# Kernel optimization log

Hardware: AMD Instinct MI355X
Metric: run time of the kernel (lower is better)

Reference implementation:

```python
import jax, jax.numpy as jnp
import numpy as np

K = 2           # top-k experts
TEMP = 1.0      # router temperature


def setup_inputs() -> dict:
    key = jax.random.key(0)
    k0, k1, k2, k3 = jax.random.split(key, 4)
    B, T, C, E = 4, 8192, 1024, 64
    x = jax.random.normal(k0, (B, T, C), dtype=jnp.float32)
    cond = jax.random.normal(k1, (B, C), dtype=jnp.float32)
    # nn.Linear weights: gate (E, C), cond_proj (C, 2C)
    Wg = jax.random.normal(k2, (E, C), dtype=jnp.float32) * 0.02
    Wc = jax.random.normal(k3, (C, 2 * C), dtype=jnp.float32) * 0.02
    return {"x": x, "cond": cond, "Wg": Wg, "Wc": Wc}


def reference(x, cond, Wg, Wc):
    B, T, C = x.shape
    E = Wg.shape[0]
    # conditioning path: broadcast cond over tokens, concat, project
    c_exp = jnp.broadcast_to(cond[:, None, :], (B, T, C))
    hc = jnp.concatenate([x, c_exp], axis=-1)          # (B,T,2C)
    h = jnp.einsum('btd,cd->btc', hc, Wc)              # (B,T,C)
    logits = jnp.einsum('btc,ec->bte', h, Wg) * (1.0 / TEMP)  # (B,T,E)
    probs = jax.nn.softmax(logits, axis=-1)
    topk_vals, idx = jax.lax.top_k(logits, K)          # (B,T,K), sorted desc
    scores = jax.nn.softmax(topk_vals, axis=-1)
    # aux stats (no_grad in torch)
    importance = jax.lax.stop_gradient(jnp.mean(probs, axis=(0, 1)))  # (E,)
    counts = jnp.zeros((E,), probs.dtype).at[idx.reshape(-1)].add(1.0)
    load = counts / jnp.clip(jnp.sum(counts), 1.0)
    load = jax.lax.stop_gradient(load)
    return (idx, scores, probs, importance, load)
```

## Files before the change

### kernel.cpp

```cpp
#include <hip/hip_runtime.h>
#include <math.h>

#define B_    4
#define T_    8192
#define C_    1024
#define E_    64
#define NTOK  (B_*T_)
#define KSEL  2

#define OFF_IDX    0
#define OFF_SCORES (NTOK*KSEL)
#define OFF_PROBS  (2*NTOK*KSEL)
#define OFF_IMP    (OFF_PROBS + NTOK*E_)
#define OFF_LOAD   (OFF_IMP + E_)

#define WS_WCOMB64 0
#define WS_HCOND64 524288
#define WS_LBIAS64 557056
#define WS_WCOMB32 559104
#define WS_LBIAS32 821248
#define WS_CNT     822272
#define WS_LIST    822784

#define REFINE_CAP 4096
#define REFINE_EPS 3e-4f

__global__ __launch_bounds__(256) void k_wcomb(const float* __restrict__ Wg,
                                               const float* __restrict__ Wc,
                                               double* __restrict__ wcomb64,
                                               float* __restrict__ wcomb32) {
    __shared__ float wg_s[64 * 65];
    __shared__ float wc_s[64 * 4];
    const int tid = threadIdx.x;
    const int e  = tid & 63;
    const int dl = tid >> 6;
    const int d  = blockIdx.x * 4 + dl;

    double acc = 0.0;
    for (int c0 = 0; c0 < C_; c0 += 64) {
        __syncthreads();
#pragma unroll
        for (int k = 0; k < 16; ++k) {
            int li = tid + k * 256;
            int el = li >> 6, cc = li & 63;
            wg_s[el * 65 + cc] = Wg[el * 1024 + c0 + cc];
        }
        {
            int cc = tid >> 2, dd = tid & 3;
            wc_s[cc * 4 + dd] = Wc[(size_t)(c0 + cc) * 2048 + blockIdx.x * 4 + dd];
        }
        __syncthreads();
#pragma unroll 4
        for (int cc = 0; cc < 64; ++cc) {
            acc += (double)wc_s[cc * 4 + dl] * (double)wg_s[e * 65 + cc];
        }
    }
    wcomb64[d * 64 + e] = acc;
    wcomb32[d * 64 + e] = (float)acc;
}

__global__ __launch_bounds__(256) void k_hcond(const float* __restrict__ cond,
                                               const float* __restrict__ Wc,
                                               double* __restrict__ hcond64) {
    int wave = (int)((blockIdx.x * blockDim.x + threadIdx.x) >> 6);
    int lane = threadIdx.x & 63;
    int b = wave >> 10;
    int c = wave & 1023;
    const float* wrow = Wc + (size_t)c * 2048 + 1024;
    const float* crow = cond + b * 1024;
    double acc = 0.0;
#pragma unroll 4
    for (int d = lane; d < 1024; d += 64)
        acc += (double)crow[d] * (double)wrow[d];
    for (int off = 32; off > 0; off >>= 1)
        acc += __shfl_down(acc, off, 64);
    if (lane == 0) hcond64[b * 1024 + c] = acc;
}

__global__ __launch_bounds__(256) void k_lbias(const double* __restrict__ hcond64,
                                               const float* __restrict__ Wg,
                                               double* __restrict__ lbias64,
                                               float* __restrict__ lbias32) {
    int wave = (int)((blockIdx.x * blockDim.x + threadIdx.x) >> 6);
    int lane = threadIdx.x & 63;
    int b = wave >> 6;
    int e = wave & 63;
    double acc = 0.0;
#pragma unroll 4
    for (int c = lane; c < 1024; c += 64)
        acc += hcond64[b * 1024 + c] * (double)Wg[e * 1024 + c];
    for (int off = 32; off > 0; off >>= 1)
        acc += __shfl_down(acc, off, 64);
    if (lane == 0) { lbias64[b * 64 + e] = acc; lbias32[b * 64 + e] = (float)acc; }
}

#define MT   64
#define XPAD 68

__global__ __launch_bounds__(256) void k_main(const float* __restrict__ x,
                                              const float* __restrict__ wcomb32,
                                              const float* __restrict__ lbias32,
                                              float* __restrict__ out,
                                              unsigned int* __restrict__ ref_cnt,
                                              int* __restrict__ ref_list) {
    __shared__ float xs[MT * XPAD];
    __shared__ float wsm[64 * 64];
    __shared__ float invs[MT];
    __shared__ unsigned int cnts[E_];

    const int tid = threadIdx.x;
    const int m_t = tid & 15;
    const int e_t = tid >> 4;
    const int token0 = blockIdx.x * MT;
    const int b = token0 / T_;

    if (tid < E_) cnts[tid] = 0;

    float4 acc[4];
#pragma unroll
    for (int i = 0; i < 4; ++i) acc[i] = make_float4(0.f, 0.f, 0.f, 0.f);

    for (int d0 = 0; d0 < C_; d0 += 64) {
        __syncthreads();
#pragma unroll
        for (int k = 0; k < 4; ++k) {
            int li = tid + k * 256;
            int r = li >> 4, c4 = (li & 15) << 2;
            float4 v = *(const float4*)&x[(size_t)(token0 + r) * C_ + d0 + c4];
            *(float4*)&xs[r * XPAD + c4] = v;
        }
#pragma unroll
        for (int k = 0; k < 4; ++k) {
            int li = tid + k * 256;
            float4 v = *(const float4*)&wcomb32[(size_t)d0 * 64 + (size_t)li * 4];
            *(float4*)&wsm[li * 4] = v;
        }
        __syncthreads();
#pragma unroll 2
        for (int j = 0; j < 64; j += 4) {
            float4 w0 = *(const float4*)&wsm[(j + 0) * 64 + e_t * 4];
            float4 w1 = *(const float4*)&wsm[(j + 1) * 64 + e_t * 4];
            float4 w2 = *(const float4*)&wsm[(j + 2) * 64 + e_t * 4];
            float4 w3 = *(const float4*)&wsm[(j + 3) * 64 + e_t * 4];
#pragma unroll
            for (int i = 0; i < 4; ++i) {
                float4 xv = *(const float4*)&xs[(m_t + 16 * i) * XPAD + j];
                acc[i].x += xv.x * w0.x; acc[i].y += xv.x * w0.y;
                acc[i].z += xv.x * w0.z; acc[i].w += xv.x * w0.w;
                acc[i].x += xv.y * w1.x; acc[i].y += xv.y * w1.y;
                acc[i].z += xv.y * w1.z; acc[i].w += xv.y * w1.w;
                acc[i].x += xv.z * w2.x; acc[i].y += xv.z * w2.y;
                acc[i].z += xv.z * w2.z; acc[i].w += xv.z * w2.w;
                acc[i].x += xv.w * w3.x; acc[i].y += xv.w * w3.y;
                acc[i].z += xv.w * w3.z; acc[i].w += xv.w * w3.w;
            }
        }
    }

    __syncthreads();
    float4 lb = *(const float4*)&lbias32[b * 64 + e_t * 4];
#pragma unroll
    for (int i = 0; i < 4; ++i) {
        int tok = m_t + 16 * i;
        float4 v = make_float4(acc[i].x + lb.x, acc[i].y + lb.y,
                               acc[i].z + lb.z, acc[i].w + lb.w);
        *(float4*)&xs[tok * XPAD + e_t * 4] = v;
    }
    __syncthreads();

    if (tid < MT) {
        const int t = tid;
        float v1 = -1e30f, v2 = -1e30f, v3 = -1e30f;
        int i1 = 0, i2 = 0;
        for (int e = 0; e < E_; ++e) {
            float l = xs[t * XPAD + e];
            if (l > v1)      { v3 = v2; v2 = v1; i2 = i1; v1 = l; i1 = e; }
            else if (l > v2) { v3 = v2; v2 = l; i2 = e; }
            else if (l > v3) { v3 = l; }
        }
        float sum = 0.f;
        for (int e = 0; e < E_; ++e) {
            float ex = __expf(xs[t * XPAD + e] - v1);
            xs[t * XPAD + e] = ex;
            sum += ex;
        }
        invs[t] = 1.0f / sum;

        const int gt = token0 + t;
        float s1 = 1.0f / (1.0f + __expf(v2 - v1));
        *(float2*)&out[OFF_IDX + (size_t)gt * 2]    = make_float2((float)i1, (float)i2);
        *(float2*)&out[OFF_SCORES + (size_t)gt * 2] = make_float2(s1, 1.0f - s1);
        atomicAdd(&cnts[i1], 1u);
        atomicAdd(&cnts[i2], 1u);

        float g12 = v1 - v2, g23 = v2 - v3;
        float g = g12 < g23 ? g12 : g23;
        if (g < REFINE_EPS) {
            unsigned int pos = atomicAdd(ref_cnt, 1u);
            if (pos < REFINE_CAP) ref_list[pos] = gt;
        }
    }
    __syncthreads();

    float* probs = out + OFF_PROBS + (size_t)token0 * E_;
#pragma unroll
    for (int k = 0; k < 4; ++k) {
        int li4 = tid + k * 256;
        int tok = li4 >> 4;
        int c4 = (li4 & 15) << 2;
        float4 ex = *(const float4*)&xs[tok * XPAD + c4];
        float inv = invs[tok];
        *(float4*)&probs[(size_t)li4 * 4] =
            make_float4(ex.x * inv, ex.y * inv, ex.z * inv, ex.w * inv);
    }

    if (tid < E_) {
        const int e = tid;
        float s = 0.f;
        for (int t = 0; t < MT; ++t) s += xs[t * XPAD + e] * invs[t];
        atomicAdd(&out[OFF_IMP + e],  s * (1.0f / (float)NTOK));
        atomicAdd(&out[OFF_LOAD + e], (float)cnts[e] * (1.0f / (float)(NTOK * KSEL)));
    }
}

__global__ __launch_bounds__(256) void k_refine(const float* __restrict__ x,
                                                const double* __restrict__ wcomb64,
                                                const double* __restrict__ lbias64,
                                                const unsigned int* __restrict__ ref_cnt,
                                                const int* __restrict__ ref_list,
                                                float* __restrict__ out) {
    int wave = (int)((blockIdx.x * blockDim.x + threadIdx.x) >> 6);
    int lane = threadIdx.x & 63;
    unsigned int n = *ref_cnt;
    if (n > REFINE_CAP) n = REFINE_CAP;
    const int nwaves = (int)((gridDim.x * blockDim.x) >> 6);

    for (unsigned int wi = wave; wi < n; wi += nwaves) {
        const int gt = ref_list[wi];
        const int b = gt / T_;
        const float* xrow = x + (size_t)gt * C_;
        double acc = lbias64[b * 64 + lane];
#pragma unroll 4
        for (int d = 0; d < C_; ++d)
            acc += (double)xrow[d] * wcomb64[d * 64 + lane];

        double v = acc; int id = lane;
        for (int off = 32; off > 0; off >>= 1) {
            double ov = __shfl_xor(v, off, 64);
            int oid   = __shfl_xor(id, off, 64);
            if (ov > v || (ov == v && oid < id)) { v = ov; id = oid; }
        }
        double v1 = v; int i1 = id;
        v = (lane == i1) ? -1e300 : acc; id = lane;
        for (int off = 32; off > 0; off >>= 1) {
            double ov = __shfl_xor(v, off, 64);
            int oid   = __shfl_xor(id, off, 64);
            if (ov > v || (ov == v && oid < id)) { v = ov; id = oid; }
        }
        double v2 = v; int i2 = id;

        if (lane == 0) {
            float s1 = (float)(1.0 / (1.0 + exp(v2 - v1)));
            *(float2*)&out[OFF_IDX + (size_t)gt * 2]    = make_float2((float)i1, (float)i2);
            *(float2*)&out[OFF_SCORES + (size_t)gt * 2] = make_float2(s1, 1.0f - s1);
        }
    }
}

extern "C" void kernel_launch(void* const* d_in, const int* in_sizes, int n_in,
                              void* d_out, int out_size, void* d_ws, size_t ws_size,
                              hipStream_t stream) {
    const float* x    = (const float*)d_in[0];
    const float* cond = (const float*)d_in[1];
    const float* Wg   = (const float*)d_in[2];
    const float* Wc   = (const float*)d_in[3];
    float* out = (float*)d_out;
    char*  ws  = (char*)d_ws;

    double* wcomb64 = (double*)(ws + WS_WCOMB64);
    double* hcond64 = (double*)(ws + WS_HCOND64);
    double* lbias64 = (double*)(ws + WS_LBIAS64);
    float*  wcomb32 = (float*)(ws + WS_WCOMB32);
    float*  lbias32 = (float*)(ws + WS_LBIAS32);
    unsigned int* ref_cnt = (unsigned int*)(ws + WS_CNT);
    int*    ref_list = (int*)(ws + WS_LIST);

    hipMemsetAsync(ref_cnt, 0, 4, stream);
    hipMemsetAsync(out + OFF_IMP, 0, 2 * E_ * sizeof(float), stream);

    k_wcomb<<<256, 256, 0, stream>>>(Wg, Wc, wcomb64, wcomb32);
    k_hcond<<<1024, 256, 0, stream>>>(cond, Wc, hcond64);
    k_lbias<<<64, 256, 0, stream>>>(hcond64, Wg, lbias64, lbias32);
    k_main<<<NTOK / MT, 256, 0, stream>>>(x, wcomb32, lbias32, out, ref_cnt, ref_list);
    k_refine<<<64, 256, 0, stream>>>(x, wcomb64, lbias64, ref_cnt, ref_list, out);
}
```

Measured before the change: 352.8 us.

## Use split-bf16 MFMA for main logits GEMM and restructure weight precompute

Measured after the change: 387.7 us. +9.9%, slower.

```diff
diff --git a/kernel.cpp b/kernel.cpp
--- a/kernel.cpp
+++ b/kernel.cpp
@@ -14,157 +14,182 @@
 #define OFF_IMP    (OFF_PROBS + NTOK*E_)
 #define OFF_LOAD   (OFF_IMP + E_)
 
-#define WS_WCOMB64 0
-#define WS_HCOND64 524288
-#define WS_LBIAS64 557056
-#define WS_WCOMB32 559104
-#define WS_LBIAS32 821248
-#define WS_CNT     822272
-#define WS_LIST    822784
-
-#define REFINE_CAP 4096
+#define WS_W64    0
+#define WS_W32    1048576
+#define WS_WTH    1310720
+#define WS_WTL    1441792
+#define WS_LB64   1572864
+#define WS_LB32   1574912
+#define WS_CNT    1575936
+#define WS_LIST   1576448
+
+#define REFINE_CAP 8192
 #define REFINE_EPS 3e-4f
 
-__global__ __launch_bounds__(256) void k_wcomb(const float* __restrict__ Wg,
-                                               const float* __restrict__ Wc,
-                                               double* __restrict__ wcomb64,
-                                               float* __restrict__ wcomb32) {
-    __shared__ float wg_s[64 * 65];
-    __shared__ float wc_s[64 * 4];
+typedef __attribute__((ext_vector_type(8))) short short8;
+typedef __attribute__((ext_vector_type(4))) float f32x4;
+
+__global__ __launch_bounds__(256) void k_comb(const float* __restrict__ Wg,
+                                              const float* __restrict__ Wc,
+                                              double* __restrict__ w64) {
+    __shared__ float wc_s[64 * 64];
+    __shared__ float wg_s[64 * 64];
+    const int tid   = threadIdx.x;
+    const int e     = tid & 63;
+    const int dg    = tid >> 6;
+    const int dtile = (blockIdx.x & 31) * 64;
+    const int cbase = (blockIdx.x >> 5) * 128;
+
+    double acc[16];
+#pragma unroll
+    for (int i = 0; i < 16; ++i) acc[i] = 0.0;
+
+    for (int cc = 0; cc < 128; cc += 64) {
+        const int c0 = cbase + cc;
+        __syncthreads();
+#pragma unroll
+        for (int k = 0; k < 4; ++k) {
+            int li = tid + k * 256;
+            int r = li >> 4, c4 = (li & 15) * 4;
+            *(float4*)&wc_s[r * 64 + c4] =
+                *(const float4*)&Wc[(size_t)(c0 + r) * 2048 + dtile + c4];
+        }
+#pragma unroll
+        for (int k = 0; k < 4; ++k) {
+            int li = tid + k * 256;
+            int r = li >> 4, c4 = (li & 15) * 4;
+            float4 v = *(const float4*)&Wg[(size_t)r * 1024 + c0 + c4];
+            wg_s[(c4 + 0) * 64 + r] = v.x;
+            wg_s[(c4 + 1) * 64 + r] = v.y;
+            wg_s[(c4 + 2) * 64 + r] = v.z;
+            wg_s[(c4 + 3) * 64 + r] = v.w;
+        }
+        __syncthreads();
+        for (int c = 0; c < 64; ++c) {
+            double wg = (double)wg_s[c * 64 + e];
+            const float* wcrow = &wc_s[c * 64 + dg * 16];
+#pragma unroll
+            for (int i = 0; i < 16; ++i)
+                acc[i] += wg * (double)wcrow[i];
+        }
+    }
+#pragma unroll
+    for (int i = 0; i < 16; ++i) {
+        double* p = &w64[(size_t)(dtile + dg * 16 + i) * 64 + e];
+#if __has_builtin(__builtin_amdgcn_global_atomic_fadd_f64)
+        unsafeAtomicAdd(p, acc[i]);
+#else
+        atomicAdd(p, acc[i]);
+#endif
+    }
+}
+
+__global__ __launch_bounds__(256) void k_finalize(const double* __restrict__ w64,
+                                                  const float* __restrict__ cond,
+                                                  float* __restrict__ wcomb32,
+                                                  short* __restrict__ wTh,
+                                                  short* __restrict__ wTl,
+                                                  double* __restrict__ lbias64,
+                                                  float* __restrict__ lbias32) {
     const int tid = threadIdx.x;
-    const int e  = tid & 63;
-    const int dl = tid >> 6;
-    const int d  = blockIdx.x * 4 + dl;
-
-    double acc = 0.0;
-    for (int c0 = 0; c0 < C_; c0 += 64) {
+    if (blockIdx.x < 64) {
+        const int e = blockIdx.x;
+        for (int d = tid; d < 1024; d += 256) {
+            float f = (float)w64[(size_t)d * 64 + e];
+            wcomb32[d * 64 + e] = f;
+            unsigned u = __float_as_uint(f);
+            short hi = (short)(u >> 16);
+            float r = f - __uint_as_float(u & 0xFFFF0000u);
+            short lo = (short)(__float_as_uint(r) >> 16);
+            wTh[e * 1024 + d] = hi;
+            wTl[e * 1024 + d] = lo;
+        }
+    } else {
+        const int b = blockIdx.x - 64;
+        const int e = tid & 63, part = tid >> 6;
+        double acc = 0.0;
+        const int d0 = part * 256;
+        for (int d = d0; d < d0 + 256; ++d)
+            acc += (double)cond[b * 1024 + d] * w64[(size_t)(1024 + d) * 64 + e];
+        __shared__ double red[256];
+        red[tid] = acc;
         __syncthreads();
-#pragma unroll
-        for (int k = 0; k < 16; ++k) {
-            int li = tid + k * 256;
-            int el = li >> 6, cc = li & 63;
-            wg_s[el * 65 + cc] = Wg[el * 1024 + c0 + cc];
-        }
-        {
-            int cc = tid >> 2, dd = tid & 3;
-            wc_s[cc * 4 + dd] = Wc[(size_t)(c0 + cc) * 2048 + blockIdx.x * 4 + dd];
-        }
-        __syncthreads();
-#pragma unroll 4
-        for (int cc = 0; cc < 64; ++cc) {
-            acc += (double)wc_s[cc * 4 + dl] * (double)wg_s[e * 65 + cc];
-        }
-    }
-    wcomb64[d * 64 + e] = acc;
-    wcomb32[d * 64 + e] = (float)acc;
-}
-
-__global__ __launch_bounds__(256) void k_hcond(const float* __restrict__ cond,
-                                               const float* __restrict__ Wc,
-                                               double* __restrict__ hcond64) {
-    int wave = (int)((blockIdx.x * blockDim.x + threadIdx.x) >> 6);
-    int lane = threadIdx.x & 63;
-    int b = wave >> 10;
-    int c = wave & 1023;
-    const float* wrow = Wc + (size_t)c * 2048 + 1024;
-    const float* crow = cond + b * 1024;
-    double acc = 0.0;
-#pragma unroll 4
-    for (int d = lane; d < 1024; d += 64)
-        acc += (double)crow[d] * (double)wrow[d];
-    for (int off = 32; off > 0; off >>= 1)
-        acc += __shfl_down(acc, off, 64);
-    if (lane == 0) hcond64[b * 1024 + c] = acc;
-}
-
-__global__ __launch_bounds__(256) void k_lbias(const double* __restrict__ hcond64,
-                                               const float* __restrict__ Wg,
-                                               double* __restrict__ lbias64,
-                                               float* __restrict__ lbias32) {
-    int wave = (int)((blockIdx.x * blockDim.x + threadIdx.x) >> 6);
-    int lane = threadIdx.x & 63;
-    int b = wave >> 6;
-    int e = wave & 63;
-    double acc = 0.0;
-#pragma unroll 4
-    for (int c = lane; c < 1024; c += 64)
-        acc += hcond64[b * 1024 + c] * (double)Wg[e * 1024 + c];
-    for (int off = 32; off > 0; off >>= 1)
-        acc += __shfl_down(acc, off, 64);
-    if (lane == 0) { lbias64[b * 64 + e] = acc; lbias32[b * 64 + e] = (float)acc; }
+        if (tid < 64) {
+            double s = red[tid] + red[tid + 64] + red[tid + 128] + red[tid + 192];
+            lbias64[b * 64 + tid] = s;
+            lbias32[b * 64 + tid] = (float)s;
+        }
+    }
+}
+
+__device__ __forceinline__ void cvt_split8(const float* __restrict__ p,
+                                           short8& h, short8& l) {
+    float4 v0 = *(const float4*)p;
+    float4 v1 = *(const float4*)(p + 4);
+    float xv[8] = {v0.x, v0.y, v0.z, v0.w, v1.x, v1.y, v1.z, v1.w};
+#pragma unroll
+    for (int j = 0; j < 8; ++j) {
+        unsigned u = __float_as_uint(xv[j]);
+        h[j] = (short)(u >> 16);
+        float r = xv[j] - __uint_as_float(u & 0xFFFF0000u);
+        l[j] = (short)(__float_as_uint(r) >> 16);
+    }
 }
 
 #define MT   64
 #define XPAD 68
 
 __global__ __launch_bounds__(256) void k_main(const float* __restrict__ x,
-                                              const float* __restrict__ wcomb32,
+                                              const short* __restrict__ wTh,
+                                              const short* __restrict__ wTl,
                                               const float* __restrict__ lbias32,
                                               float* __restrict__ out,
                                               unsigned int* __restrict__ ref_cnt,
                                               int* __restrict__ ref_list) {
     __shared__ float xs[MT * XPAD];
-    __shared__ float wsm[64 * 64];
     __shared__ float invs[MT];
     __shared__ unsigned int cnts[E_];
 
-    const int tid = threadIdx.x;
-    const int m_t = tid & 15;
-    const int e_t = tid >> 4;
+    const int tid    = threadIdx.x;
+    const int wid    = tid >> 6;
+    const int lane   = tid & 63;
+    const int nn     = lane & 15;
+    const int q8     = (lane >> 4) * 8;
     const int token0 = blockIdx.x * MT;
-    const int b = token0 / T_;
+    const int t0     = token0 + wid * 16;
+    const int b      = token0 / T_;
 
     if (tid < E_) cnts[tid] = 0;
 
-    float4 acc[4];
-#pragma unroll
-    for (int i = 0; i < 4; ++i) acc[i] = make_float4(0.f, 0.f, 0.f, 0.f);
-
-    for (int d0 = 0; d0 < C_; d0 += 64) {
-        __syncthreads();
-#pragma unroll
-        for (int k = 0; k < 4; ++k) {
-            int li = tid + k * 256;
-            int r = li >> 4, c4 = (li & 15) << 2;
-            float4 v = *(const float4*)&x[(size_t)(token0 + r) * C_ + d0 + c4];
-            *(float4*)&xs[r * XPAD + c4] = v;
-        }
-#pragma unroll
-        for (int k = 0; k < 4; ++k) {
-            int li = tid + k * 256;
-            float4 v = *(const float4*)&wcomb32[(size_t)d0 * 64 + (size_t)li * 4];
-            *(float4*)&wsm[li * 4] = v;
-        }
-        __syncthreads();
+    f32x4 acc[4];
+#pragma unroll
+    for (int et = 0; et < 4; ++et) acc[et] = (f32x4){0.f, 0.f, 0.f, 0.f};
+
+    const float* aptr = x + (size_t)(t0 + nn) * 1024 + q8;
 #pragma unroll 2
-        for (int j = 0; j < 64; j += 4) {
-            float4 w0 = *(const float4*)&wsm[(j + 0) * 64 + e_t * 4];
-            float4 w1 = *(const float4*)&wsm[(j + 1) * 64 + e_t * 4];
-            float4 w2 = *(const float4*)&wsm[(j + 2) * 64 + e_t * 4];
-            float4 w3 = *(const float4*)&wsm[(j + 3) * 64 + e_t * 4];
-#pragma unroll
-            for (int i = 0; i < 4; ++i) {
-                float4 xv = *(const float4*)&xs[(m_t + 16 * i) * XPAD + j];
-                acc[i].x += xv.x * w0.x; acc[i].y += xv.x * w0.y;
-                acc[i].z += xv.x * w0.z; acc[i].w += xv.x * w0.w;
-                acc[i].x += xv.y * w1.x; acc[i].y += xv.y * w1.y;
-                acc[i].z += xv.y * w1.z; acc[i].w += xv.y * w1.w;
-                acc[i].x += xv.z * w2.x; acc[i].y += xv.z * w2.y;
-                acc[i].z += xv.z * w2.z; acc[i].w += xv.z * w2.w;
-                acc[i].x += xv.w * w3.x; acc[i].y += xv.w * w3.y;
-                acc[i].z += xv.w * w3.z; acc[i].w += xv.w * w3.w;
-            }
-        }
-    }
-
-    __syncthreads();
-    float4 lb = *(const float4*)&lbias32[b * 64 + e_t * 4];
-#pragma unroll
-    for (int i = 0; i < 4; ++i) {
-        int tok = m_t + 16 * i;
-        float4 v = make_float4(acc[i].x + lb.x, acc[i].y + lb.y,
-                               acc[i].z + lb.z, acc[i].w + lb.w);
-        *(float4*)&xs[tok * XPAD + e_t * 4] = v;
+    for (int k0 = 0; k0 < 1024; k0 += 32) {
+        short8 ah, al;
+        cvt_split8(aptr + k0, ah, al);
+#pragma unroll
+        for (int et = 0; et < 4; ++et) {
+            const size_t boff = (size_t)(et * 16 + nn) * 1024 + k0 + q8;
+            short8 bh = *(const short8*)(wTh + boff);
+            short8 bl = *(const short8*)(wTl + boff);
+            acc[et] = __builtin_amdgcn_mfma_f32_16x16x32_bf16(ah, bh, acc[et], 0, 0, 0);
+            acc[et] = __builtin_amdgcn_mfma_f32_16x16x32_bf16(ah, bl, acc[et], 0, 0, 0);
+            acc[et] = __builtin_amdgcn_mfma_f32_16x16x32_bf16(al, bh, acc[et], 0, 0, 0);
+        }
+    }
+
+    const int q4 = (lane >> 4) * 4;
+#pragma unroll
+    for (int et = 0; et < 4; ++et) {
+        float lb = lbias32[b * 64 + et * 16 + nn];
+#pragma unroll
+        for (int r = 0; r < 4; ++r) {
+            int tok = wid * 16 + q4 + r;
+            xs[tok * XPAD + et * 16 + nn] = acc[et][r] + lb;
+        }
     }
     __syncthreads();
 
@@ -224,7 +249,7 @@
 }
 
 __global__ __launch_bounds__(256) void k_refine(const float* __restrict__ x,
-                                                const double* __restrict__ wcomb64,
+                                                const float* __restrict__ wcomb32,
                                                 const double* __restrict__ lbias64,
                                                 const unsigned int* __restrict__ ref_cnt,
                                                 const int* __restrict__ ref_list,
@@ -239,10 +264,14 @@
         const int gt = ref_list[wi];
         const int b = gt / T_;
         const float* xrow = x + (size_t)gt * C_;
-        double acc = lbias64[b * 64 + lane];
-#pragma unroll 4
-        for (int d = 0; d < C_; ++d)
-            acc += (double)xrow[d] * wcomb64[d * 64 + lane];
+        double a0 = 0.0, a1 = 0.0, a2 = 0.0, a3 = 0.0;
+        for (int d = 0; d < C_; d += 4) {
+            a0 += (double)xrow[d + 0] * (double)wcomb32[(d + 0) * 64 + lane];
+            a1 += (double)xrow[d + 1] * (double)wcomb32[(d + 1) * 64 + lane];
+            a2 += (double)xrow[d + 2] * (double)wcomb32[(d + 2) * 64 + lane];
+            a3 += (double)xrow[d + 3] * (double)wcomb32[(d + 3) * 64 + lane];
+        }
+        double acc = ((a0 + a1) + (a2 + a3)) + lbias64[b * 64 + lane];
 
         double v = acc; int id = lane;
         for (int off = 32; off > 0; off >>= 1) {
@@ -277,20 +306,21 @@
     float* out = (float*)d_out;
     char*  ws  = (char*)d_ws;
 
-    double* wcomb64 = (double*)(ws + WS_WCOMB64);
-    double* hcond64 = (double*)(ws + WS_HCOND64);
-    double* lbias64 = (double*)(ws + WS_LBIAS64);
-    float*  wcomb32 = (float*)(ws + WS_WCOMB32);
-    float*  lbias32 = (float*)(ws + WS_LBIAS32);
+    double* w64     = (double*)(ws + WS_W64);
+    float*  wcomb32 = (float*)(ws + WS_W32);
+    short*  wTh     = (short*)(ws + WS_WTH);
+    short*  wTl     = (short*)(ws + WS_WTL);
+    double* lbias64 = (double*)(ws + WS_LB64);
+    float*  lbias32 = (float*)(ws + WS_LB32);
     unsigned int* ref_cnt = (unsigned int*)(ws + WS_CNT);
     int*    ref_list = (int*)(ws + WS_LIST);
 
+    hipMemsetAsync(w64, 0, 2048 * 64 * sizeof(double), stream);
     hipMemsetAsync(ref_cnt, 0, 4, stream);
     hipMemsetAsync(out + OFF_IMP, 0, 2 * E_ * sizeof(float), stream);
 
-    k_wcomb<<<256, 256, 0, stream>>>(Wg, Wc, wcomb64, wcomb32);
-    k_hcond<<<1024, 256, 0, stream>>>(cond, Wc, hcond64);
-    k_lbias<<<64, 256, 0, stream>>>(hcond64, Wg, lbias64, lbias32);
-    k_main<<<NTOK / MT, 256, 0, stream>>>(x, wcomb32, lbias32, out, ref_cnt, ref_list);
-    k_refine<<<64, 256, 0, stream>>>(x, wcomb64, lbias64, ref_cnt, ref_list, out);
-}
+    k_comb<<<256, 256, 0, stream>>>(Wg, Wc, w64);
+    k_finalize<<<68, 256, 0, stream>>>(w64, cond, wcomb32, wTh, wTl, lbias64, lbias32);
+    k_main<<<NTOK / MT, 256, 0, stream>>>(x, wTh, wTl, lbias32, out, ref_cnt, ref_list);
+    k_refine<<<256, 256, 0, stream>>>(x, wcomb32, lbias64, ref_cnt, ref_list, out);
+}
```
